# Performance work log

Hardware: AMD Instinct MI355X
Metric: run time of the kernel (lower is better)

## Reference

```python
import jax, jax.numpy as jnp
import numpy as np

DIM = 256
HEAD_DIM = 64
NH = DIM // HEAD_DIM
PS = 2  # fine patch size
EPS = 1e-5


def _conv(x, w, b, stride, pad):
    y = jax.lax.conv_general_dilated(x, w, (stride, stride), ((pad, pad), (pad, pad)),
                                     dimension_numbers=('NCHW', 'OIHW', 'NCHW'))
    return y + b[None, :, None, None]


def _bn(x, g, b, m, v):
    s = g * jax.lax.rsqrt(v + EPS)
    return x * s[None, :, None, None] + (b - m * s)[None, :, None, None]


def setup_inputs() -> dict:
    key = jax.random.key(0)
    ks = jax.random.split(key, 24)
    C = DIM
    d = {}
    d['x'] = jax.random.normal(ks[0], (8, C, 64, 64), jnp.float32)
    # Downsample conv (C->C, k=4, s=2, p=1), torch OIHW layout
    d['w_down'] = jax.random.normal(ks[1], (C, C, 4, 4), jnp.float32) * 0.02
    d['b_down'] = jax.random.normal(ks[2], (C,), jnp.float32) * 0.02
    # coarse to_qkv Linear(64 -> 192), stored as [in, out]
    d['w_qkv_c'] = jax.random.normal(ks[3], (HEAD_DIM, 3 * HEAD_DIM), jnp.float32) * 0.05
    d['b_qkv_c'] = jax.random.normal(ks[4], (3 * HEAD_DIM,), jnp.float32) * 0.02
    # Upsample ConvTranspose2d (torch [in, out, kH, kW] layout)
    d['w_up'] = jax.random.normal(ks[5], (C, C, 4, 4), jnp.float32) * 0.02
    d['b_up'] = jax.random.normal(ks[6], (C,), jnp.float32) * 0.02
    # fine to_qkv Linear(64 -> 192)
    d['w_qkv_f'] = jax.random.normal(ks[7], (HEAD_DIM, 3 * HEAD_DIM), jnp.float32) * 0.05
    d['b_qkv_f'] = jax.random.normal(ks[8], (3 * HEAD_DIM,), jnp.float32) * 0.02
    # DWConv: depthwise 3x3 (groups=C) -> BN -> relu6 -> pointwise 1x1 -> BN -> relu6
    d['w_dw'] = jax.random.normal(ks[9], (C, 1, 3, 3), jnp.float32) * 0.1
    d['bn_dw_g'] = jax.random.uniform(ks[10], (C,), jnp.float32) * 0.5 + 0.75
    d['bn_dw_b'] = jax.random.normal(ks[11], (C,), jnp.float32) * 0.1
    d['bn_dw_m'] = jax.random.normal(ks[12], (C,), jnp.float32) * 0.1
    d['bn_dw_v'] = jax.random.uniform(ks[13], (C,), jnp.float32) + 0.5
    d['w_pw'] = jax.random.normal(ks[14], (C, C, 1, 1), jnp.float32) * 0.05
    d['bn_pw_g'] = jax.random.uniform(ks[15], (C,), jnp.float32) * 0.5 + 0.75
    d['bn_pw_b'] = jax.random.normal(ks[16], (C,), jnp.float32) * 0.1
    d['bn_pw_m'] = jax.random.normal(ks[17], (C,), jnp.float32) * 0.1
    d['bn_pw_v'] = jax.random.uniform(ks[18], (C,), jnp.float32) + 0.5
    return d


def reference(x, w_down, b_down, w_qkv_c, b_qkv_c, w_up, b_up, w_qkv_f, b_qkv_f,
              w_dw, bn_dw_g, bn_dw_b, bn_dw_m, bn_dw_v,
              w_pw, bn_pw_g, bn_pw_b, bn_pw_m, bn_pw_v):
    B, C, H, W = x.shape
    nh, hd = C // HEAD_DIM, HEAD_DIM
    scale = hd ** -0.5

    # ---- CoarseSelfAttention ----
    xd = _conv(x, w_down, b_down, 2, 1)           # [B,C,h,w]
    h, w = xd.shape[2], xd.shape[3]
    P = h * w
    tok = xd.reshape(B, nh, hd, P).transpose(0, 1, 3, 2)   # [B,nh,P,hd]
    q, k, v = jnp.split(tok @ w_qkv_c + b_qkv_c, 3, axis=-1)
    attn = jax.nn.softmax(jnp.einsum('bhqd,bhkd->bhqk', q, k) * scale, axis=-1)
    coarse_score = attn.sum(axis=-2)               # [B,nh,P]
    kf = max(1, P // 4)
    top_k = jax.lax.top_k(coarse_score, kf)[1]     # [B,nh,kf]
    out = jnp.einsum('bhqk,bhkd->bhqd', attn, v)
    out = out.transpose(0, 1, 3, 2).reshape(B, C, h, w)
    # ConvTranspose2d(k=4,s=2,p=1) as lhs-dilated conv with flipped/transposed kernel
    wt = jnp.flip(w_up, (2, 3)).transpose(1, 0, 2, 3)
    coarse = jax.lax.conv_general_dilated(out, wt, (1, 1), ((2, 2), (2, 2)),
                                          lhs_dilation=(2, 2),
                                          dimension_numbers=('NCHW', 'OIHW', 'NCHW'))
    coarse = coarse + b_up[None, :, None, None]
    # F.interpolate to (H,W) is identity here: upsample exactly restores HxW

    # ---- TopkSelfAttention ----
    ph, pw = H // PS, W // PS                      # ph*pw == P
    xh = coarse.reshape(B, nh, hd, ph, PS, pw, PS)
    patches = xh.transpose(0, 1, 2, 3, 5, 4, 6).reshape(B, nh, hd, ph * pw, PS, PS)
    idx = jnp.broadcast_to(top_k[:, :, None, :, None, None], (B, nh, hd, kf, PS, PS))
    sel = jnp.take_along_axis(patches, idx, axis=3)        # [B,nh,hd,kf,PS,PS]
    tokf = sel.reshape(B, nh, hd, kf, PS * PS).transpose(0, 1, 3, 4, 2)
    tokf = tokf.reshape(B, nh, kf * PS * PS, hd)
    qf, kk, vf = jnp.split(tokf @ w_qkv_f + b_qkv_f, 3, axis=-1)
    attnf = jax.nn.softmax(jnp.einsum('bhqd,bhkd->bhqk', qf, kk) * scale, axis=-1)
    outf = jnp.einsum('bhqk,bhkd->bhqd', attnf, vf)
    outf = outf.reshape(B, nh, kf, PS * PS, hd).transpose(0, 1, 2, 4, 3)
    outf = outf.reshape(B, nh, kf, hd, PS, PS)     # [B,nh,kf,hd,PS,PS]
    # scatter selected patches back into zeros (topk indices are unique per b,h)
    res = jnp.zeros((B, nh, ph * pw, hd, PS, PS), x.dtype)
    bi = jnp.arange(B)[:, None, None]
    hi = jnp.arange(nh)[None, :, None]
    res = res.at[bi, hi, top_k].set(outf)
    res = res.transpose(0, 1, 3, 2, 4, 5).reshape(B, nh, hd, ph, pw, PS, PS)
    region = res.transpose(0, 1, 2, 3, 5, 4, 6).reshape(B, C, H, W)

    y = coarse + region

    # ---- DWConv feed-forward ----
    yd = jax.lax.conv_general_dilated(y, w_dw, (1, 1), ((1, 1), (1, 1)),
                                      feature_group_count=C,
                                      dimension_numbers=('NCHW', 'OIHW', 'NCHW'))
    yd = jnp.clip(_bn(yd, bn_dw_g, bn_dw_b, bn_dw_m, bn_dw_v), 0.0, 6.0)
    yp = jax.lax.conv_general_dilated(yd, w_pw, (1, 1), ((0, 0), (0, 0)),
                                      dimension_numbers=('NCHW', 'OIHW', 'NCHW'))
    yp = jnp.clip(_bn(yp, bn_pw_g, bn_pw_b, bn_pw_m, bn_pw_v), 0.0, 6.0)
    return yp
```

## Files before the change

### kernel.cpp

```cpp
#include <hip/hip_runtime.h>
#include <cstdint>
#include <cstddef>


#define EPS_ 1e-5f

typedef short bf16x8_t __attribute__((ext_vector_type(8)));
typedef float f32x4_t __attribute__((ext_vector_type(4)));
#define MFMA16(a, b, c) __builtin_amdgcn_mfma_f32_16x16x32_bf16(a, b, c, 0, 0, 0)

__device__ __forceinline__ void cvt1(float f, unsigned short& h, unsigned short& l) {
  unsigned u = __float_as_uint(f);
  unsigned r = u + 0x7FFFu + ((u >> 16) & 1u);
  h = (unsigned short)(r >> 16);
  float lo = f - __uint_as_float(r & 0xFFFF0000u);
  l = (unsigned short)(__float_as_uint(lo) >> 16);
}
__device__ __forceinline__ unsigned cvtpack(float f) {
  unsigned short h, l;
  cvt1(f, h, l);
  return (unsigned)h | ((unsigned)l << 16);
}
__device__ __forceinline__ void cvt2(float f0, float f1, unsigned& hpack, unsigned& lpack) {
  unsigned u0 = __float_as_uint(f0), u1 = __float_as_uint(f1);
  unsigned r0 = u0 + 0x7FFFu + ((u0 >> 16) & 1u);
  unsigned r1 = u1 + 0x7FFFu + ((u1 >> 16) & 1u);
  hpack = (r0 >> 16) | (r1 & 0xFFFF0000u);
  float l0 = f0 - __uint_as_float(r0 & 0xFFFF0000u);
  float l1 = f1 - __uint_as_float(r1 & 0xFFFF0000u);
  lpack = (__float_as_uint(l0) >> 16) | (__float_as_uint(l1) & 0xFFFF0000u);
}
__device__ __forceinline__ unsigned pk_h(unsigned a, unsigned b) {
  return (a & 0xFFFFu) | (b << 16);
}
__device__ __forceinline__ unsigned pk_l(unsigned a, unsigned b) {
  return (a >> 16) | (b & 0xFFFF0000u);
}

__global__ __launch_bounds__(256) void k_pad_x(
    const float* __restrict__ x, unsigned* __restrict__ xphl) {
  const int plane = blockIdx.x;
  const float* src = x + (size_t)plane * 4096;
  unsigned* dst = xphl + (size_t)plane * 4488;
  for (int e = threadIdx.x; e < 4356; e += 256) {
    int r = e / 66, cc = e - r * 66;
    float v = 0.f;
    if (r >= 1 && r <= 64 && cc >= 1 && cc <= 64) v = src[(r - 1) * 64 + (cc - 1)];
    dst[r * 68 + cc] = cvtpack(v);
  }
}

__global__ __launch_bounds__(256) void k_cvt_wdown(
    const float* __restrict__ w, unsigned short* __restrict__ wh,
    unsigned short* __restrict__ wl) {
  int e = blockIdx.x * 256 + threadIdx.x;
  cvt1(w[e], wh[e], wl[e]);
}

__global__ __launch_bounds__(256) void k_cvt_wqkv(
    const float* __restrict__ wq, unsigned short* __restrict__ wh,
    unsigned short* __restrict__ wl) {
  int e = blockIdx.x * 256 + threadIdx.x;
  int col = e >> 6, d = e & 63;
  float f = wq[d * 192 + col];
  if (col < 64) f *= 0.125f;
  cvt1(f, wh[e], wl[e]);
}

__global__ __launch_bounds__(256) void k_cvt_wup(
    const float* __restrict__ w_up, unsigned short* __restrict__ wth,
    unsigned short* __restrict__ wtl) {
  int e = blockIdx.x * 256 + threadIdx.x;
  int kp = e & 1023, oc = (e >> 10) & 255, c = e >> 18;
  int tap = kp >> 8, ic = kp & 255;
  int tk = tap >> 1, txi = tap & 1;
  int ry = c >> 1, rx = c & 1;
  int ky = (1 - ry) + 2 * tk, kx = (1 - rx) + 2 * txi;
  cvt1(w_up[((size_t)(ic * 256 + oc) * 4 + ky) * 4 + kx], wth[e], wtl[e]);
}

__global__ __launch_bounds__(256) void k_cvt_wpw(
    const float* __restrict__ w, unsigned short* __restrict__ wh,
    unsigned short* __restrict__ wl) {
  int e = blockIdx.x * 256 + threadIdx.x;
  cvt1(w[e], wh[e], wl[e]);
}

__device__ __forceinline__ void mfma_chunk(
    const unsigned short (*Ah)[72], const unsigned short (*Al)[72],
    const unsigned short (*Bh)[72], const unsigned short (*Bl)[72],
    f32x4_t (&acc)[4], int wm, int lane) {
  const int l16 = lane & 15, quad = lane >> 4;
#pragma unroll
  for (int ks = 0; ks < 2; ++ks) {
    int ko = ks * 32 + quad * 8;
    bf16x8_t ah = *(const bf16x8_t*)&Ah[wm + l16][ko];
    bf16x8_t al = *(const bf16x8_t*)&Al[wm + l16][ko];
#pragma unroll
    for (int nt = 0; nt < 4; ++nt) {
      bf16x8_t bh = *(const bf16x8_t*)&Bh[nt * 16 + l16][ko];
      bf16x8_t bl = *(const bf16x8_t*)&Bl[nt * 16 + l16][ko];
      acc[nt] = MFMA16(ah, bh, acc[nt]);
      acc[nt] = MFMA16(ah, bl, acc[nt]);
      acc[nt] = MFMA16(al, bh, acc[nt]);
    }
  }
}

__device__ __forceinline__ void mfma_chunk_regB(
    const unsigned short (*Ah)[72], const unsigned short (*Al)[72],
    const bf16x8_t (&bh)[2][4], const bf16x8_t (&bl)[2][4],
    f32x4_t (&acc)[4], int wm, int lane) {
  const int l16 = lane & 15, quad = lane >> 4;
#pragma unroll
  for (int ks = 0; ks < 2; ++ks) {
    int ko = ks * 32 + quad * 8;
    bf16x8_t ah = *(const bf16x8_t*)&Ah[wm + l16][ko];
    bf16x8_t al = *(const bf16x8_t*)&Al[wm + l16][ko];
#pragma unroll
    for (int nt = 0; nt < 4; ++nt) {
      acc[nt] = MFMA16(ah, bh[ks][nt], acc[nt]);
      acc[nt] = MFMA16(ah, bl[ks][nt], acc[nt]);
      acc[nt] = MFMA16(al, bh[ks][nt], acc[nt]);
    }
  }
}

__device__ __forceinline__ void mfma_tile2x2(
    const unsigned short (*Ah)[72], const unsigned short (*Al)[72],
    const unsigned short (*Bh)[72], const unsigned short (*Bl)[72],
    f32x4_t (&acc)[2][2], int wm, int wn, int lane) {
  const int l16 = lane & 15, quad = lane >> 4;
#pragma unroll
  for (int ks = 0; ks < 2; ++ks) {
    int ko = ks * 32 + quad * 8;
    bf16x8_t ah[2], al[2];
#pragma unroll
    for (int mt = 0; mt < 2; ++mt) {
      ah[mt] = *(const bf16x8_t*)&Ah[wm + mt * 16 + l16][ko];
      al[mt] = *(const bf16x8_t*)&Al[wm + mt * 16 + l16][ko];
    }
#pragma unroll
    for (int nt = 0; nt < 2; ++nt) {
      bf16x8_t bh = *(const bf16x8_t*)&Bh[wn + nt * 16 + l16][ko];
      bf16x8_t bl = *(const bf16x8_t*)&Bl[wn + nt * 16 + l16][ko];
#pragma unroll
      for (int mt = 0; mt < 2; ++mt) {
        acc[mt][nt] = MFMA16(ah[mt], bh, acc[mt][nt]);
        acc[mt][nt] = MFMA16(ah[mt], bl, acc[mt][nt]);
        acc[mt][nt] = MFMA16(al[mt], bh, acc[mt][nt]);
      }
    }
  }
}

__device__ __forceinline__ void mfma_tile2x4(
    const unsigned short (*Ah)[72], const unsigned short (*Al)[72],
    const unsigned short (*Bh)[72], const unsigned short (*Bl)[72],
    f32x4_t (&acc)[2][4], int wm, int wn, int lane) {
  const int l16 = lane & 15, quad = lane >> 4;
#pragma unroll
  for (int ks = 0; ks < 2; ++ks) {
    int ko = ks * 32 + quad * 8;
    bf16x8_t ah[2], al[2];
#pragma unroll
    for (int mt = 0; mt < 2; ++mt) {
      ah[mt] = *(const bf16x8_t*)&Ah[wm + mt * 16 + l16][ko];
      al[mt] = *(const bf16x8_t*)&Al[wm + mt * 16 + l16][ko];
    }
#pragma unroll
    for (int nt = 0; nt < 4; ++nt) {
      bf16x8_t bh = *(const bf16x8_t*)&Bh[wn + nt * 16 + l16][ko];
      bf16x8_t bl = *(const bf16x8_t*)&Bl[wn + nt * 16 + l16][ko];
#pragma unroll
      for (int mt = 0; mt < 2; ++mt) {
        acc[mt][nt] = MFMA16(ah[mt], bh, acc[mt][nt]);
        acc[mt][nt] = MFMA16(ah[mt], bl, acc[mt][nt]);
        acc[mt][nt] = MFMA16(al[mt], bh, acc[mt][nt]);
      }
    }
  }
}

__global__ __launch_bounds__(256) void k_conv_down_mfma(
    const unsigned* __restrict__ xphl, const unsigned short* __restrict__ wdh,
    const unsigned short* __restrict__ wdl, const float* __restrict__ bias,
    unsigned* __restrict__ xdhl) {
  __shared__ unsigned short Ah[64][72], Al[64][72], Bh[64][72], Bl[64][72];
  const int t = threadIdx.x;
  const int pix0 = blockIdx.x * 64, oc0 = blockIdx.y * 64;
  const int bimg = pix0 >> 10, pos = pix0 & 1023;
  const int pl = t & 63, icg = t >> 6;
  const int rem = (pix0 + pl) & 1023;
  const int oy = rem >> 5, ox = rem & 31;
  const unsigned* xb = xphl + ((size_t)bimg * 256 + icg) * 4488 + (oy * 2) * 68 + ox * 2;
  const int wave = t >> 6, lane = t & 63, l16 = lane & 15, quad = lane >> 4;
  const int wm = (wave & 1) * 32, wn = (wave >> 1) * 32;
  const int ar = t >> 2, ac = (t & 3) * 16;
  const unsigned short* wra = wdh + (size_t)(oc0 + ar) * 4096 + ac;
  const unsigned short* wrl = wdl + (size_t)(oc0 + ar) * 4096 + ac;
  f32x4_t acc[2][2] = {};
  bf16x8_t a0, a1, a2, a3;
  uint2 u01[4], u23[4];
  a0 = *(const bf16x8_t*)(wra);
  a1 = *(const bf16x8_t*)(wra + 8);
  a2 = *(const bf16x8_t*)(wrl);
  a3 = *(const bf16x8_t*)(wrl + 8);
#pragma unroll
  for (int r = 0; r < 4; ++r) {
    u01[r] = *(const uint2*)(xb + r * 68);
    u23[r] = *(const uint2*)(xb + r * 68 + 2);
  }
  for (int kb = 0; kb < 4096; kb += 64) {
    unsigned hp[8], lp[8];
#pragma unroll
    for (int r = 0; r < 4; ++r) {
      hp[2 * r]     = pk_h(u01[r].x, u01[r].y);
      lp[2 * r]     = pk_l(u01[r].x, u01[r].y);
      hp[2 * r + 1] = pk_h(u23[r].x, u23[r].y);
      lp[2 * r + 1] = pk_l(u23[r].x, u23[r].y);
    }
    __syncthreads();
    *(bf16x8_t*)&Ah[ar][ac] = a0;
    *(bf16x8_t*)&Ah[ar][ac + 8] = a1;
    *(bf16x8_t*)&Al[ar][ac] = a2;
    *(bf16x8_t*)&Al[ar][ac + 8] = a3;
    *(uint4*)&Bh[pl][icg * 16] = make_uint4(hp[0], hp[1], hp[2], hp[3]);
    *(uint4*)&Bh[pl][icg * 16 + 8] = make_uint4(hp[4], hp[5], hp[6], hp[7]);
    *(uint4*)&Bl[pl][icg * 16] = make_uint4(lp[0], lp[1], lp[2], lp[3]);
    *(uint4*)&Bl[pl][icg * 16 + 8] = make_uint4(lp[4], lp[5], lp[6], lp[7]);
    if (kb + 64 < 4096) {
      xb += 4 * 4488;
      a0 = *(const bf16x8_t*)(wra + kb + 64);
      a1 = *(const bf16x8_t*)(wra + kb + 64 + 8);
      a2 = *(const bf16x8_t*)(wrl + kb + 64);
      a3 = *(const bf16x8_t*)(wrl + kb + 64 + 8);
#pragma unroll
      for (int r = 0; r < 4; ++r) {
        u01[r] = *(const uint2*)(xb + r * 68);
        u23[r] = *(const uint2*)(xb + r * 68 + 2);
      }
    }
    __syncthreads();
    mfma_tile2x2(Ah, Al, Bh, Bl, acc, wm, wn, lane);
  }
#pragma unroll
  for (int mt = 0; mt < 2; ++mt)
#pragma unroll
    for (int r = 0; r < 4; ++r) {
      int oc = oc0 + wm + mt * 16 + quad * 4 + r;
      float bv = bias[oc];
#pragma unroll
      for (int nt = 0; nt < 2; ++nt)
        xdhl[((size_t)(bimg * 256 + oc)) * 1024 + pos + wn + nt * 16 + l16] =
            cvtpack(acc[mt][nt][r] + bv);
    }
}

template <int MODE>
__global__ __launch_bounds__(256) void k_qkv_mfma(
    const unsigned* __restrict__ srcp, const float* __restrict__ srcf,
    const unsigned short* __restrict__ wh, const unsigned short* __restrict__ wl,
    const float* __restrict__ bq, const int* __restrict__ topk,
    unsigned short* __restrict__ qh, unsigned short* __restrict__ ql,
    unsigned short* __restrict__ kh, unsigned short* __restrict__ kl,
    unsigned short* __restrict__ vth, unsigned short* __restrict__ vtl) {
  __shared__ unsigned short Ah[64][72], Al[64][72];
  const int t = threadIdx.x;
  const int tok0 = blockIdx.x * 64;
  const int pair = blockIdx.y;
  const int b = pair >> 2, h = pair & 3;
  const int tokl = t & 63, dg = t >> 6;
  unsigned hp[8], lp[8];
  if (MODE == 0) {
    const unsigned* base = srcp + ((size_t)(b * 256 + h * 64 + dg * 16)) * 1024 + tok0 + tokl;
    unsigned u[16];
#pragma unroll
    for (int j = 0; j < 16; ++j) u[j] = base[(size_t)j * 1024];
#pragma unroll
    for (int j = 0; j < 8; ++j) {
      hp[j] = pk_h(u[2 * j], u[2 * j + 1]);
      lp[j] = pk_l(u[2 * j], u[2 * j + 1]);
    }
  } else {
    int tok = tok0 + tokl;
    int pp = topk[pair * 256 + (tok >> 2)];
    int py = (tok >> 1) & 1, px = tok & 1;
    int ry = (pp >> 5) * 2 + py, rx = (pp & 31) * 2 + px;
    const float* base = srcf + ((size_t)(b * 256 + h * 64 + dg * 16)) * 4096 + ry * 64 + rx;
    float fv[16];
#pragma unroll
    for (int j = 0; j < 16; ++j) fv[j] = base[(size_t)j * 4096];
#pragma unroll
    for (int j = 0; j < 8; ++j) cvt2(fv[2 * j], fv[2 * j + 1], hp[j], lp[j]);
  }
  *(uint4*)&Ah[tokl][dg * 16] = make_uint4(hp[0], hp[1], hp[2], hp[3]);
  *(uint4*)&Ah[tokl][dg * 16 + 8] = make_uint4(hp[4], hp[5], hp[6], hp[7]);
  *(uint4*)&Al[tokl][dg * 16] = make_uint4(lp[0], lp[1], lp[2], lp[3]);
  *(uint4*)&Al[tokl][dg * 16 + 8] = make_uint4(lp[4], lp[5], lp[6], lp[7]);
  __syncthreads();
  const int wave = t >> 6, lane = t & 63, l16 = lane & 15, quad = lane >> 4;
  f32x4_t acc[4][3] = {};
#pragma unroll
  for (int ks = 0; ks < 2; ++ks) {
    int ko = ks * 32 + quad * 8;
    bf16x8_t bh0[3], bl0[3];
#pragma unroll
    for (int nt = 0; nt < 3; ++nt) {
      int col = wave * 48 + nt * 16 + l16;
      bh0[nt] = *(const bf16x8_t*)(wh + col * 64 + ko);
      bl0[nt] = *(const bf16x8_t*)(wl + col * 64 + ko);
    }
#pragma unroll
    for (int mt = 0; mt < 4; ++mt) {
      bf16x8_t ah = *(const bf16x8_t*)&Ah[mt * 16 + l16][ko];
      bf16x8_t al = *(const bf16x8_t*)&Al[mt * 16 + l16][ko];
#pragma unroll
      for (int nt = 0; nt < 3; ++nt) {
        acc[mt][nt] = MFMA16(ah, bh0[nt], acc[mt][nt]);
        acc[mt][nt] = MFMA16(ah, bl0[nt], acc[mt][nt]);
        acc[mt][nt] = MFMA16(al, bh0[nt], acc[mt][nt]);
      }
    }
  }
#pragma unroll
  for (int nt = 0; nt < 3; ++nt) {
    int col = wave * 48 + nt * 16 + l16;
    float bqv = bq[col];
    if (col < 64) bqv *= 0.125f;
#pragma unroll
    for (int mt = 0; mt < 4; ++mt) {
#pragma unroll
      for (int r = 0; r < 4; ++r) {
        int tok = tok0 + mt * 16 + quad * 4 + r;
        float val = acc[mt][nt][r] + bqv;
        unsigned short hh, ll;
        cvt1(val, hh, ll);
        if (col < 64) {
          size_t o = ((size_t)pair * 1024 + tok) * 64 + col;
          qh[o] = hh; ql[o] = ll;
        } else if (col < 128) {
          size_t o = ((size_t)pair * 1024 + tok) * 64 + (col - 64);
          kh[o] = hh; kl[o] = ll;
        } else {
          size_t o = ((size_t)pair * 64 + (col - 128)) * 1024 + tok;
          vth[o] = hh; vtl[o] = ll;
        }
      }
    }
  }
}

__global__ __launch_bounds__(256, 2) void k_attn_coarse(
    const unsigned short* __restrict__ qh, const unsigned short* __restrict__ ql,
    const unsigned short* __restrict__ kh, const unsigned short* __restrict__ kl,
    const unsigned short* __restrict__ vth, const unsigned short* __restrict__ vtl,
    float* __restrict__ score, unsigned* __restrict__ outc) {
  __shared__ __align__(16) unsigned short Kb[2][64][72];
  __shared__ __align__(16) unsigned short Vb[2][64][72];
  __shared__ __align__(16) unsigned short Pb[2][64][72];
  __shared__ float mlW[4][2][64];
  __shared__ float mC[64], lC[64];
  __shared__ float colsum[1024];
  const int t = threadIdx.x;
  const int q0 = blockIdx.x * 64;
  const int pair = blockIdx.y;
  const int wave = t >> 6, lane = t & 63;
  const int l16 = lane & 15, quad = lane >> 4;
  const int wm = wave * 16;
  const int sr = t >> 3, skc = (t & 7) * 8;

  const size_t qbase = ((size_t)pair * 1024 + q0) * 64;
  bf16x8_t qh_r[2][4], ql_r[2][4];
#pragma unroll
  for (int ks = 0; ks < 2; ++ks)
#pragma unroll
    for (int nt = 0; nt < 4; ++nt) {
      int row = nt * 16 + l16, col = ks * 32 + quad * 8;
      qh_r[ks][nt] = *(const bf16x8_t*)(qh + qbase + (size_t)row * 64 + col);
      ql_r[ks][nt] = *(const bf16x8_t*)(ql + qbase + (size_t)row * 64 + col);
    }
#pragma unroll
  for (int i = 0; i < 4; ++i) colsum[t + i * 256] = 0.f;

  const size_t kmbase = (size_t)pair * 1024 * 64;
  const size_t vbase = (size_t)pair * 64 * 1024;

  bf16x8_t pk0[2], pk1[2];
#pragma unroll
  for (int i = 0; i < 2; ++i) {
    int r = sr + i * 32;
    pk0[i] = *(const bf16x8_t*)(kh + kmbase + (size_t)r * 64 + skc);
    pk1[i] = *(const bf16x8_t*)(kl + kmbase + (size_t)r * 64 + skc);
  }

  float mrun[4] = {-1e30f, -1e30f, -1e30f, -1e30f};
  float lrun[4] = {0.f, 0.f, 0.f, 0.f};
// ... 141 lines not shown
    const unsigned short* __restrict__ kh, const unsigned short* __restrict__ kl,
    const unsigned short* __restrict__ vth, const unsigned short* __restrict__ vtl,
    float* __restrict__ outf) {
  __shared__ __align__(16) unsigned short Kb[2][64][72];
  __shared__ __align__(16) unsigned short Vb[2][64][72];
  __shared__ __align__(16) unsigned short Pb[2][64][72];
  __shared__ float m_run[64], l_run[64], alphaS[64];
  __shared__ float mWc[4][64], sWc[4][64];
  const int t = threadIdx.x;
  const int q0 = blockIdx.x * 64;
  const int pair = blockIdx.y;
  const int wave = t >> 6, lane = t & 63;
  const int l16 = lane & 15, quad = lane >> 4;
  const int wm = wave * 16;
  const int sr = t >> 3, skc = (t & 7) * 8;

  const size_t qbase = ((size_t)pair * 1024 + q0) * 64;
  bf16x8_t qh_r[2][4], ql_r[2][4];
#pragma unroll
  for (int ks = 0; ks < 2; ++ks)
#pragma unroll
    for (int nt = 0; nt < 4; ++nt) {
      int row = nt * 16 + l16, col = ks * 32 + quad * 8;
      qh_r[ks][nt] = *(const bf16x8_t*)(qh + qbase + (size_t)row * 64 + col);
      ql_r[ks][nt] = *(const bf16x8_t*)(ql + qbase + (size_t)row * 64 + col);
    }
  if (t < 64) { m_run[t] = -1e30f; l_run[t] = 0.f; }

  const size_t kmbase = (size_t)pair * 1024 * 64;
  const size_t vbase = (size_t)pair * 64 * 1024;

  bf16x8_t pk0[2], pk1[2], pv0[2], pv1[2];
#pragma unroll
  for (int i = 0; i < 2; ++i) {
    int r = sr + i * 32;
    pk0[i] = *(const bf16x8_t*)(kh + kmbase + (size_t)r * 64 + skc);
    pk1[i] = *(const bf16x8_t*)(kl + kmbase + (size_t)r * 64 + skc);
    pv0[i] = *(const bf16x8_t*)(vth + vbase + (size_t)r * 1024 + skc);
    pv1[i] = *(const bf16x8_t*)(vtl + vbase + (size_t)r * 1024 + skc);
  }

  f32x4_t accO[4] = {};
  for (int kb = 0; kb < 1024; kb += 64) {
    __syncthreads();
#pragma unroll
    for (int i = 0; i < 2; ++i) {
      int r = sr + i * 32;
      *(bf16x8_t*)&Kb[0][r][skc] = pk0[i];
      *(bf16x8_t*)&Kb[1][r][skc] = pk1[i];
      *(bf16x8_t*)&Vb[0][r][skc] = pv0[i];
      *(bf16x8_t*)&Vb[1][r][skc] = pv1[i];
    }
    if (kb + 64 < 1024) {
#pragma unroll
      for (int i = 0; i < 2; ++i) {
        int r = sr + i * 32;
        pk0[i] = *(const bf16x8_t*)(kh + kmbase + (size_t)(kb + 64 + r) * 64 + skc);
        pk1[i] = *(const bf16x8_t*)(kl + kmbase + (size_t)(kb + 64 + r) * 64 + skc);
        pv0[i] = *(const bf16x8_t*)(vth + vbase + (size_t)r * 1024 + kb + 64 + skc);
        pv1[i] = *(const bf16x8_t*)(vtl + vbase + (size_t)r * 1024 + kb + 64 + skc);
      }
    }
    __syncthreads();
    f32x4_t acc[4] = {};
    mfma_chunk_regB(Kb[0], Kb[1], qh_r, ql_r, acc, wm, lane);
#pragma unroll
    for (int nt = 0; nt < 4; ++nt) {
      float m0 = fmaxf(fmaxf(acc[nt][0], acc[nt][1]), fmaxf(acc[nt][2], acc[nt][3]));
      m0 = fmaxf(m0, __shfl_xor(m0, 16));
      m0 = fmaxf(m0, __shfl_xor(m0, 32));
      if (quad == 0) mWc[wave][nt * 16 + l16] = m0;
    }
    __syncthreads();
    if (t < 64) {
      float mn = fmaxf(fmaxf(fmaxf(mWc[0][t], mWc[1][t]), fmaxf(mWc[2][t], mWc[3][t])),
                       m_run[t]);
      alphaS[t] = __expf(m_run[t] - mn);
      m_run[t] = mn;
    }
    __syncthreads();
    float P[4][4];
#pragma unroll
    for (int nt = 0; nt < 4; ++nt) {
      float mn = m_run[nt * 16 + l16];
#pragma unroll
      for (int r = 0; r < 4; ++r) P[nt][r] = __expf(acc[nt][r] - mn);
      float s0 = P[nt][0] + P[nt][1] + P[nt][2] + P[nt][3];
      s0 += __shfl_xor(s0, 16);
      s0 += __shfl_xor(s0, 32);
      if (quad == 0) sWc[wave][nt * 16 + l16] = s0;
      unsigned h01, l01, h23, l23;
      cvt2(P[nt][0], P[nt][1], h01, l01);
      cvt2(P[nt][2], P[nt][3], h23, l23);
      *(uint2*)&Pb[0][nt * 16 + l16][wm + quad * 4] = make_uint2(h01, h23);
      *(uint2*)&Pb[1][nt * 16 + l16][wm + quad * 4] = make_uint2(l01, l23);
    }
#pragma unroll
    for (int r = 0; r < 4; ++r) {
      float a = alphaS[wm + quad * 4 + r];
#pragma unroll
      for (int nt = 0; nt < 4; ++nt) accO[nt][r] *= a;
    }
    __syncthreads();
    if (t < 64)
      l_run[t] = l_run[t] * alphaS[t] + (sWc[0][t] + sWc[1][t] + sWc[2][t] + sWc[3][t]);
    mfma_chunk(Pb[0], Pb[1], Vb[0], Vb[1], accO, wm, lane);
  }
  __syncthreads();
#pragma unroll
  for (int r = 0; r < 4; ++r) {
    float invl = 1.0f / l_run[wm + quad * 4 + r];
    int qm = q0 + wm + quad * 4 + r;
#pragma unroll
    for (int nt = 0; nt < 4; ++nt)
      outf[((size_t)pair * 1024 + qm) * 64 + nt * 16 + l16] = accO[nt][r] * invl;
  }
}

__global__ __launch_bounds__(256) void k_topk(
    const float* __restrict__ score, int* __restrict__ idx) {
  __shared__ unsigned long long key[1024];
  const int pair = blockIdx.x;
  const int t = threadIdx.x;
#pragma unroll
  for (int j = 0; j < 4; ++j) {
    int i = t + j * 256;
    unsigned u = __float_as_uint(score[pair * 1024 + i]);
    u = u ^ ((u & 0x80000000u) ? 0xFFFFFFFFu : 0x80000000u);
    u = ~u;
    key[i] = ((unsigned long long)u << 32) | (unsigned)i;
  }
  __syncthreads();
  for (int k = 2; k <= 1024; k <<= 1) {
    for (int j = k >> 1; j > 0; j >>= 1) {
      for (int w = 0; w < 4; ++w) {
        int i = t + w * 256;
        int l = i ^ j;
        if (l > i) {
          bool up = ((i & k) == 0);
          unsigned long long a = key[i], b = key[l];
          if ((a > b) == up) { key[i] = b; key[l] = a; }
        }
      }
      __syncthreads();
    }
  }
  idx[pair * 256 + t] = (int)(key[t] & 0xFFFFFFFFu);
}

__global__ __launch_bounds__(256) void k_convT_mfma(
    const unsigned* __restrict__ inp, const unsigned short* __restrict__ wth,
    const unsigned short* __restrict__ wtl, const float* __restrict__ bias,
    float* __restrict__ out) {
  __shared__ unsigned short Ah[64][72], Al[64][72];
  __shared__ unsigned short Bh[128][72], Bl[128][72];
  const int t = threadIdx.x;
  const int pix0 = blockIdx.x * 128;
  const int oc0 = blockIdx.y * 64;
  const int cls = blockIdx.z;
  const int ry = cls >> 1, rx = cls & 1;
  const int b = pix0 >> 10;
  const int wave = t >> 6, lane = t & 63;
  const int l16 = lane & 15, quad = lane >> 4;
  const int wm = (wave & 1) * 32, wn = (wave >> 1) * 64;
  const int pl = t & 127, icg = t >> 7;
  const int remg = (pix0 + pl) & 1023;
  const int tyy = remg >> 5, txx = remg & 31;
  const int ar = t >> 2, ac = (t & 3) * 16;
  const size_t wbase = ((size_t)cls * 256 + oc0 + ar) * 1024 + ac;
  f32x4_t acc[2][4] = {};
  bf16x8_t a0, a1, a2, a3;
  unsigned u[32];
  {
    const int iy = tyy + ry + 1, ix = txx + rx + 1;
    const unsigned* p = inp + (size_t)(b * 256 + icg * 32) * 1156 + iy * 34 + ix;
#pragma unroll
    for (int j = 0; j < 32; ++j) u[j] = p[(size_t)j * 1156];
    a0 = *(const bf16x8_t*)(wth + wbase);
    a1 = *(const bf16x8_t*)(wth + wbase + 8);
    a2 = *(const bf16x8_t*)(wtl + wbase);
    a3 = *(const bf16x8_t*)(wtl + wbase + 8);
  }
  for (int kb = 0; kb < 1024; kb += 64) {
    unsigned hp[16], lpk[16];
#pragma unroll
    for (int j = 0; j < 16; ++j) {
      hp[j] = pk_h(u[2 * j], u[2 * j + 1]);
      lpk[j] = pk_l(u[2 * j], u[2 * j + 1]);
    }
    __syncthreads();
    *(bf16x8_t*)&Ah[ar][ac] = a0;
    *(bf16x8_t*)&Ah[ar][ac + 8] = a1;
    *(bf16x8_t*)&Al[ar][ac] = a2;
    *(bf16x8_t*)&Al[ar][ac + 8] = a3;
    {
      int kc = icg * 32;
      *(uint4*)&Bh[pl][kc] = make_uint4(hp[0], hp[1], hp[2], hp[3]);
      *(uint4*)&Bh[pl][kc + 8] = make_uint4(hp[4], hp[5], hp[6], hp[7]);
      *(uint4*)&Bh[pl][kc + 16] = make_uint4(hp[8], hp[9], hp[10], hp[11]);
      *(uint4*)&Bh[pl][kc + 24] = make_uint4(hp[12], hp[13], hp[14], hp[15]);
      *(uint4*)&Bl[pl][kc] = make_uint4(lpk[0], lpk[1], lpk[2], lpk[3]);
      *(uint4*)&Bl[pl][kc + 8] = make_uint4(lpk[4], lpk[5], lpk[6], lpk[7]);
      *(uint4*)&Bl[pl][kc + 16] = make_uint4(lpk[8], lpk[9], lpk[10], lpk[11]);
      *(uint4*)&Bl[pl][kc + 24] = make_uint4(lpk[12], lpk[13], lpk[14], lpk[15]);
    }
    if (kb + 64 < 1024) {
      const int kn = kb + 64;
      const int tap = kn >> 8, ic0 = kn & 255;
      const int tk = tap >> 1, txi = tap & 1;
      const int iy = tyy + ry + 1 - tk, ix = txx + rx + 1 - txi;
      const unsigned* p = inp + (size_t)(b * 256 + ic0 + icg * 32) * 1156 + iy * 34 + ix;
#pragma unroll
      for (int j = 0; j < 32; ++j) u[j] = p[(size_t)j * 1156];
      a0 = *(const bf16x8_t*)(wth + wbase + kn);
      a1 = *(const bf16x8_t*)(wth + wbase + kn + 8);
      a2 = *(const bf16x8_t*)(wtl + wbase + kn);
      a3 = *(const bf16x8_t*)(wtl + wbase + kn + 8);
    }
    __syncthreads();
    mfma_tile2x4(Ah, Al, Bh, Bl, acc, wm, wn, lane);
  }
#pragma unroll
  for (int mt = 0; mt < 2; ++mt)
#pragma unroll
    for (int r = 0; r < 4; ++r) {
      int oc = oc0 + wm + mt * 16 + quad * 4 + r;
      float bvs = bias[oc];
#pragma unroll
      for (int nt = 0; nt < 4; ++nt) {
        int pix = pix0 + wn + nt * 16 + l16;
        int rem2 = pix & 1023;
        int y = (rem2 >> 5) * 2 + ry, xx = (rem2 & 31) * 2 + rx;
        out[((size_t)(b * 256 + oc) * 64 + y) * 64 + xx] = acc[mt][nt][r] + bvs;
      }
    }
}

__global__ __launch_bounds__(256) void k_scatter(
    const float* __restrict__ outf, const int* __restrict__ idx,
    float* __restrict__ y) {
  int g = blockIdx.x * 256 + threadIdx.x;
  int pair = g >> 16;
  int rem = g & 65535;
  int tok = rem >> 6, d = rem & 63;
  int b = pair >> 2, h = pair & 3;
  int pp = idx[pair * 256 + (tok >> 2)];
  int py = (tok >> 1) & 1, px = tok & 1;
  int ry = (pp >> 5) * 2 + py, rx = (pp & 31) * 2 + px;
  y[((size_t)(b * 256 + h * 64 + d) * 64 + ry) * 64 + rx] += outf[g];
}

__global__ __launch_bounds__(256) void k_dwconv(
    const float* __restrict__ y, const float* __restrict__ wdw,
    const float* __restrict__ g, const float* __restrict__ bb,
    const float* __restrict__ m, const float* __restrict__ vv,
    unsigned* __restrict__ ydhl) {
  int gi = blockIdx.x * 256 + threadIdx.x;
  int x = gi & 63, yy = (gi >> 6) & 63, ch = (gi >> 12) & 255, b = gi >> 20;
  const float* plane = y + (size_t)(b * 256 + ch) * 4096;
  const float* wc = wdw + ch * 9;
  float s = 0.f;
#pragma unroll
  for (int ky = 0; ky < 3; ++ky) {
    int iy = yy + ky - 1;
    if (iy < 0 || iy >= 64) continue;
#pragma unroll
    for (int kx = 0; kx < 3; ++kx) {
      int ix = x + kx - 1;
      if (ix < 0 || ix >= 64) continue;
      s = fmaf(plane[iy * 64 + ix], wc[ky * 3 + kx], s);
    }
  }
  float sc = g[ch] * rsqrtf(vv[ch] + EPS_);
  float val = s * sc + (bb[ch] - m[ch] * sc);
  ydhl[gi] = cvtpack(fminf(fmaxf(val, 0.f), 6.f));
}

__global__ __launch_bounds__(256) void k_pw_mfma(
    const unsigned* __restrict__ ydhl, const unsigned short* __restrict__ wh,
    const unsigned short* __restrict__ wl, const float* __restrict__ g,
    const float* __restrict__ bb, const float* __restrict__ m,
    const float* __restrict__ vv, float* __restrict__ out) {
  __shared__ unsigned short Ah[64][72], Al[64][72];
  __shared__ unsigned short Bh[128][72], Bl[128][72];
  const int t = threadIdx.x;
  const int pix0 = blockIdx.x * 128;
  const int oc0 = blockIdx.y * 64;
  const int b = pix0 >> 12, pos0 = pix0 & 4095;
  const int wave = t >> 6, lane = t & 63;
  const int l16 = lane & 15, quad = lane >> 4;
  const int wm = (wave & 1) * 32, wn = (wave >> 1) * 64;
  const int pl = t & 127, icg = t >> 7;
  const int ar = t >> 2, ac = (t & 3) * 16;
  f32x4_t acc[2][4] = {};
  bf16x8_t a0, a1, a2, a3;
  unsigned u[32];
  {
    const unsigned* p = ydhl + (size_t)(b * 256 + icg * 32) * 4096 + pos0 + pl;
#pragma unroll
    for (int j = 0; j < 32; ++j) u[j] = p[(size_t)j * 4096];
    a0 = *(const bf16x8_t*)(wh + (size_t)(oc0 + ar) * 256 + ac);
    a1 = *(const bf16x8_t*)(wh + (size_t)(oc0 + ar) * 256 + ac + 8);
    a2 = *(const bf16x8_t*)(wl + (size_t)(oc0 + ar) * 256 + ac);
    a3 = *(const bf16x8_t*)(wl + (size_t)(oc0 + ar) * 256 + ac + 8);
  }
  for (int kb = 0; kb < 256; kb += 64) {
    unsigned hp[16], lpk[16];
#pragma unroll
    for (int j = 0; j < 16; ++j) {
      hp[j] = pk_h(u[2 * j], u[2 * j + 1]);
      lpk[j] = pk_l(u[2 * j], u[2 * j + 1]);
    }
    __syncthreads();
    *(bf16x8_t*)&Ah[ar][ac] = a0;
    *(bf16x8_t*)&Ah[ar][ac + 8] = a1;
    *(bf16x8_t*)&Al[ar][ac] = a2;
    *(bf16x8_t*)&Al[ar][ac + 8] = a3;
    {
      int kc = icg * 32;
      *(uint4*)&Bh[pl][kc] = make_uint4(hp[0], hp[1], hp[2], hp[3]);
      *(uint4*)&Bh[pl][kc + 8] = make_uint4(hp[4], hp[5], hp[6], hp[7]);
      *(uint4*)&Bh[pl][kc + 16] = make_uint4(hp[8], hp[9], hp[10], hp[11]);
      *(uint4*)&Bh[pl][kc + 24] = make_uint4(hp[12], hp[13], hp[14], hp[15]);
      *(uint4*)&Bl[pl][kc] = make_uint4(lpk[0], lpk[1], lpk[2], lpk[3]);
      *(uint4*)&Bl[pl][kc + 8] = make_uint4(lpk[4], lpk[5], lpk[6], lpk[7]);
      *(uint4*)&Bl[pl][kc + 16] = make_uint4(lpk[8], lpk[9], lpk[10], lpk[11]);
      *(uint4*)&Bl[pl][kc + 24] = make_uint4(lpk[12], lpk[13], lpk[14], lpk[15]);
    }
    if (kb + 64 < 256) {
      const int kn = kb + 64;
      const unsigned* p = ydhl + (size_t)(b * 256 + kn + icg * 32) * 4096 + pos0 + pl;
#pragma unroll
      for (int j = 0; j < 32; ++j) u[j] = p[(size_t)j * 4096];
      a0 = *(const bf16x8_t*)(wh + (size_t)(oc0 + ar) * 256 + kn + ac);
      a1 = *(const bf16x8_t*)(wh + (size_t)(oc0 + ar) * 256 + kn + ac + 8);
      a2 = *(const bf16x8_t*)(wl + (size_t)(oc0 + ar) * 256 + kn + ac);
      a3 = *(const bf16x8_t*)(wl + (size_t)(oc0 + ar) * 256 + kn + ac + 8);
    }
    __syncthreads();
    mfma_tile2x4(Ah, Al, Bh, Bl, acc, wm, wn, lane);
  }
#pragma unroll
  for (int mt = 0; mt < 2; ++mt)
#pragma unroll
    for (int r = 0; r < 4; ++r) {
      int oc = oc0 + wm + mt * 16 + quad * 4 + r;
      float sc = g[oc] * rsqrtf(vv[oc] + EPS_);
      float off = bb[oc] - m[oc] * sc;
#pragma unroll
      for (int nt = 0; nt < 4; ++nt) {
        int pix = pos0 + wn + nt * 16 + l16;
        float val = fminf(fmaxf(acc[mt][nt][r] * sc + off, 0.f), 6.f);
        out[(size_t)(b * 256 + oc) * 4096 + pix] = val;
      }
    }
}

extern "C" void kernel_launch(void* const* d_in, const int* in_sizes, int n_in,
                              void* d_out, int out_size, void* d_ws, size_t ws_size,
                              hipStream_t stream) {
  (void)in_sizes; (void)n_in; (void)out_size; (void)ws_size;
  const float* x       = (const float*)d_in[0];
  const float* w_down  = (const float*)d_in[1];
  const float* b_down  = (const float*)d_in[2];
  const float* w_qkv_c = (const float*)d_in[3];
  const float* b_qkv_c = (const float*)d_in[4];
  const float* w_up    = (const float*)d_in[5];
  const float* b_up    = (const float*)d_in[6];
  const float* w_qkv_f = (const float*)d_in[7];
  const float* b_qkv_f = (const float*)d_in[8];
  const float* w_dw    = (const float*)d_in[9];
  const float* bn_dw_g = (const float*)d_in[10];
  const float* bn_dw_b = (const float*)d_in[11];
  const float* bn_dw_m = (const float*)d_in[12];
  const float* bn_dw_v = (const float*)d_in[13];
  const float* w_pw    = (const float*)d_in[14];
  const float* bn_pw_g = (const float*)d_in[15];
  const float* bn_pw_b = (const float*)d_in[16];
  const float* bn_pw_m = (const float*)d_in[17];
  const float* bn_pw_v = (const float*)d_in[18];

  float* ws = (float*)d_ws;
  unsigned*       xphl   = (unsigned*)ws;
  unsigned*       ydhl   = (unsigned*)ws;
  unsigned short* qh     = (unsigned short*)(ws + 33554432);
  unsigned short* ql     = (unsigned short*)(ws + 34603008);
  unsigned short* kh     = (unsigned short*)(ws + 35651584);
  unsigned short* kl     = (unsigned short*)(ws + 36700160);
  unsigned short* vth    = (unsigned short*)(ws + 37748736);
  unsigned short* vtl    = (unsigned short*)(ws + 38797312);
  unsigned*       xdhl   = (unsigned*)(ws + 39845888);
  unsigned*       outcphl= (unsigned*)(ws + 41943040);
  float*          coarse = ws + 44310528;
  float*          outf   = ws + 52699136;
  float*          score  = ws + 54796288;
  unsigned short* wdh    = (unsigned short*)(ws + 54829056);
  unsigned short* wdl    = (unsigned short*)(ws + 55353344);
  unsigned short* wt_hi  = (unsigned short*)(ws + 55877632);
  unsigned short* wt_lo  = (unsigned short*)(ws + 56401920);
  unsigned short* wpw_hi = (unsigned short*)(ws + 56926208);
  unsigned short* wpw_lo = (unsigned short*)(ws + 56958976);
  unsigned short* wqh_c  = (unsigned short*)(ws + 56991744);
  unsigned short* wql_c  = (unsigned short*)(ws + 56997888);
  unsigned short* wqh_f  = (unsigned short*)(ws + 57004032);
  unsigned short* wql_f  = (unsigned short*)(ws + 57010176);
  int*            idx    = (int*)(ws + 57016320);

  hipMemsetAsync(score, 0, 32768 * sizeof(float), stream);
  hipMemsetAsync(outcphl, 0, (size_t)2367488 * sizeof(unsigned), stream);
  k_pad_x<<<2048, 256, 0, stream>>>(x, xphl);
  k_cvt_wdown<<<4096, 256, 0, stream>>>(w_down, wdh, wdl);
  k_cvt_wqkv<<<48, 256, 0, stream>>>(w_qkv_c, wqh_c, wql_c);
  k_cvt_wqkv<<<48, 256, 0, stream>>>(w_qkv_f, wqh_f, wql_f);
  k_cvt_wup<<<4096, 256, 0, stream>>>(w_up, wt_hi, wt_lo);
  k_cvt_wpw<<<256, 256, 0, stream>>>(w_pw, wpw_hi, wpw_lo);

  k_conv_down_mfma<<<dim3(128, 4), 256, 0, stream>>>(xphl, wdh, wdl, b_down, xdhl);
  k_qkv_mfma<0><<<dim3(16, 32), 256, 0, stream>>>(xdhl, nullptr, wqh_c, wql_c, b_qkv_c,
                                                  nullptr, qh, ql, kh, kl, vth, vtl);
  k_attn_coarse<<<dim3(16, 32), 256, 0, stream>>>(qh, ql, kh, kl, vth, vtl, score, outcphl);
  k_topk<<<32, 256, 0, stream>>>(score, idx);
  k_convT_mfma<<<dim3(64, 4, 4), 256, 0, stream>>>(outcphl, wt_hi, wt_lo, b_up, coarse);

  k_qkv_mfma<1><<<dim3(16, 32), 256, 0, stream>>>(nullptr, coarse, wqh_f, wql_f, b_qkv_f,
                                                  idx, qh, ql, kh, kl, vth, vtl);
  k_attn_fine<<<dim3(16, 32), 256, 0, stream>>>(qh, ql, kh, kl, vth, vtl, outf);
  k_scatter<<<8192, 256, 0, stream>>>(outf, idx, coarse);
  k_dwconv<<<32768, 256, 0, stream>>>(coarse, w_dw, bn_dw_g, bn_dw_b, bn_dw_m, bn_dw_v, ydhl);
  k_pw_mfma<<<dim3(256, 4), 256, 0, stream>>>(ydhl, wpw_hi, wpw_lo, bn_pw_g, bn_pw_b,
                                              bn_pw_m, bn_pw_v, (float*)d_out);
}
```

Measured before the change: 598.7 us.

## Double-buffer LDS in MFMA conv GEMMs and shrink convT/pointwise pixel tiles

Converts the down-conv, transposed-conv and pointwise-conv GEMM loops to ping-pong shared-memory buffers, removing one barrier per k-step. ConvT and pointwise kernels also drop from 128-pixel to 64-pixel tiles with 2x2 MFMA per wave, doubling grid size and reducing registers. The trade is higher LDS usage per block and less operand reuse per tile.

```diff
diff --git a/kernel.cpp b/kernel.cpp
--- a/kernel.cpp
+++ b/kernel.cpp
@@ -154,39 +154,12 @@
   }
 }
 
-__device__ __forceinline__ void mfma_tile2x4(
-    const unsigned short (*Ah)[72], const unsigned short (*Al)[72],
-    const unsigned short (*Bh)[72], const unsigned short (*Bl)[72],
-    f32x4_t (&acc)[2][4], int wm, int wn, int lane) {
-  const int l16 = lane & 15, quad = lane >> 4;
-#pragma unroll
-  for (int ks = 0; ks < 2; ++ks) {
-    int ko = ks * 32 + quad * 8;
-    bf16x8_t ah[2], al[2];
-#pragma unroll
-    for (int mt = 0; mt < 2; ++mt) {
-      ah[mt] = *(const bf16x8_t*)&Ah[wm + mt * 16 + l16][ko];
-      al[mt] = *(const bf16x8_t*)&Al[wm + mt * 16 + l16][ko];
-    }
-#pragma unroll
-    for (int nt = 0; nt < 4; ++nt) {
-      bf16x8_t bh = *(const bf16x8_t*)&Bh[wn + nt * 16 + l16][ko];
-      bf16x8_t bl = *(const bf16x8_t*)&Bl[wn + nt * 16 + l16][ko];
-#pragma unroll
-      for (int mt = 0; mt < 2; ++mt) {
-        acc[mt][nt] = MFMA16(ah[mt], bh, acc[mt][nt]);
-        acc[mt][nt] = MFMA16(ah[mt], bl, acc[mt][nt]);
-        acc[mt][nt] = MFMA16(al[mt], bh, acc[mt][nt]);
-      }
-    }
-  }
-}
-
 __global__ __launch_bounds__(256) void k_conv_down_mfma(
     const unsigned* __restrict__ xphl, const unsigned short* __restrict__ wdh,
     const unsigned short* __restrict__ wdl, const float* __restrict__ bias,
     unsigned* __restrict__ xdhl) {
-  __shared__ unsigned short Ah[64][72], Al[64][72], Bh[64][72], Bl[64][72];
+  __shared__ unsigned short Ah[2][64][72], Al[2][64][72];
+  __shared__ unsigned short Bh[2][64][72], Bl[2][64][72];
   const int t = threadIdx.x;
   const int pix0 = blockIdx.x * 64, oc0 = blockIdx.y * 64;
   const int bimg = pix0 >> 10, pos = pix0 & 1023;
@@ -211,6 +184,7 @@
     u01[r] = *(const uint2*)(xb + r * 68);
     u23[r] = *(const uint2*)(xb + r * 68 + 2);
   }
+  int cur = 0;
   for (int kb = 0; kb < 4096; kb += 64) {
     unsigned hp[8], lp[8];
 #pragma unroll
@@ -220,15 +194,14 @@
       hp[2 * r + 1] = pk_h(u23[r].x, u23[r].y);
       lp[2 * r + 1] = pk_l(u23[r].x, u23[r].y);
     }
-    __syncthreads();
-    *(bf16x8_t*)&Ah[ar][ac] = a0;
-    *(bf16x8_t*)&Ah[ar][ac + 8] = a1;
-    *(bf16x8_t*)&Al[ar][ac] = a2;
-    *(bf16x8_t*)&Al[ar][ac + 8] = a3;
-    *(uint4*)&Bh[pl][icg * 16] = make_uint4(hp[0], hp[1], hp[2], hp[3]);
-    *(uint4*)&Bh[pl][icg * 16 + 8] = make_uint4(hp[4], hp[5], hp[6], hp[7]);
-    *(uint4*)&Bl[pl][icg * 16] = make_uint4(lp[0], lp[1], lp[2], lp[3]);
-    *(uint4*)&Bl[pl][icg * 16 + 8] = make_uint4(lp[4], lp[5], lp[6], lp[7]);
+    *(bf16x8_t*)&Ah[cur][ar][ac] = a0;
+    *(bf16x8_t*)&Ah[cur][ar][ac + 8] = a1;
+    *(bf16x8_t*)&Al[cur][ar][ac] = a2;
+    *(bf16x8_t*)&Al[cur][ar][ac + 8] = a3;
+    *(uint4*)&Bh[cur][pl][icg * 16] = make_uint4(hp[0], hp[1], hp[2], hp[3]);
+    *(uint4*)&Bh[cur][pl][icg * 16 + 8] = make_uint4(hp[4], hp[5], hp[6], hp[7]);
+    *(uint4*)&Bl[cur][pl][icg * 16] = make_uint4(lp[0], lp[1], lp[2], lp[3]);
+    *(uint4*)&Bl[cur][pl][icg * 16 + 8] = make_uint4(lp[4], lp[5], lp[6], lp[7]);
     if (kb + 64 < 4096) {
       xb += 4 * 4488;
       a0 = *(const bf16x8_t*)(wra + kb + 64);
@@ -242,7 +215,8 @@
       }
     }
     __syncthreads();
-    mfma_tile2x2(Ah, Al, Bh, Bl, acc, wm, wn, lane);
+    mfma_tile2x2(Ah[cur], Al[cur], Bh[cur], Bl[cur], acc, wm, wn, lane);
+    cur ^= 1;
   }
 #pragma unroll
   for (int mt = 0; mt < 2; ++mt)
@@ -690,73 +664,67 @@
     const unsigned* __restrict__ inp, const unsigned short* __restrict__ wth,
     const unsigned short* __restrict__ wtl, const float* __restrict__ bias,
     float* __restrict__ out) {
-  __shared__ unsigned short Ah[64][72], Al[64][72];
-  __shared__ unsigned short Bh[128][72], Bl[128][72];
+  __shared__ unsigned short Ah[2][64][72], Al[2][64][72];
+  __shared__ unsigned short Bh[2][64][72], Bl[2][64][72];
   const int t = threadIdx.x;
-  const int pix0 = blockIdx.x * 128;
+  const int pix0 = blockIdx.x * 64;
   const int oc0 = blockIdx.y * 64;
   const int cls = blockIdx.z;
   const int ry = cls >> 1, rx = cls & 1;
   const int b = pix0 >> 10;
   const int wave = t >> 6, lane = t & 63;
   const int l16 = lane & 15, quad = lane >> 4;
-  const int wm = (wave & 1) * 32, wn = (wave >> 1) * 64;
-  const int pl = t & 127, icg = t >> 7;
+  const int wm = (wave & 1) * 32, wn = (wave >> 1) * 32;
+  const int pl = t & 63, icg = t >> 6;
   const int remg = (pix0 + pl) & 1023;
   const int tyy = remg >> 5, txx = remg & 31;
   const int ar = t >> 2, ac = (t & 3) * 16;
   const size_t wbase = ((size_t)cls * 256 + oc0 + ar) * 1024 + ac;
-  f32x4_t acc[2][4] = {};
+  f32x4_t acc[2][2] = {};
   bf16x8_t a0, a1, a2, a3;
-  unsigned u[32];
+  unsigned u[16];
   {
     const int iy = tyy + ry + 1, ix = txx + rx + 1;
-    const unsigned* p = inp + (size_t)(b * 256 + icg * 32) * 1156 + iy * 34 + ix;
-#pragma unroll
-    for (int j = 0; j < 32; ++j) u[j] = p[(size_t)j * 1156];
+    const unsigned* p = inp + (size_t)(b * 256 + icg * 16) * 1156 + iy * 34 + ix;
+#pragma unroll
+    for (int j = 0; j < 16; ++j) u[j] = p[(size_t)j * 1156];
     a0 = *(const bf16x8_t*)(wth + wbase);
     a1 = *(const bf16x8_t*)(wth + wbase + 8);
     a2 = *(const bf16x8_t*)(wtl + wbase);
     a3 = *(const bf16x8_t*)(wtl + wbase + 8);
   }
+  int cur = 0;
   for (int kb = 0; kb < 1024; kb += 64) {
-    unsigned hp[16], lpk[16];
-#pragma unroll
-    for (int j = 0; j < 16; ++j) {
+    unsigned hp[8], lpk[8];
+#pragma unroll
+    for (int j = 0; j < 8; ++j) {
       hp[j] = pk_h(u[2 * j], u[2 * j + 1]);
       lpk[j] = pk_l(u[2 * j], u[2 * j + 1]);
     }
-    __syncthreads();
-    *(bf16x8_t*)&Ah[ar][ac] = a0;
-    *(bf16x8_t*)&Ah[ar][ac + 8] = a1;
-    *(bf16x8_t*)&Al[ar][ac] = a2;
-    *(bf16x8_t*)&Al[ar][ac + 8] = a3;
-    {
-      int kc = icg * 32;
-      *(uint4*)&Bh[pl][kc] = make_uint4(hp[0], hp[1], hp[2], hp[3]);
-      *(uint4*)&Bh[pl][kc + 8] = make_uint4(hp[4], hp[5], hp[6], hp[7]);
-      *(uint4*)&Bh[pl][kc + 16] = make_uint4(hp[8], hp[9], hp[10], hp[11]);
-      *(uint4*)&Bh[pl][kc + 24] = make_uint4(hp[12], hp[13], hp[14], hp[15]);
-      *(uint4*)&Bl[pl][kc] = make_uint4(lpk[0], lpk[1], lpk[2], lpk[3]);
-      *(uint4*)&Bl[pl][kc + 8] = make_uint4(lpk[4], lpk[5], lpk[6], lpk[7]);
-      *(uint4*)&Bl[pl][kc + 16] = make_uint4(lpk[8], lpk[9], lpk[10], lpk[11]);
-      *(uint4*)&Bl[pl][kc + 24] = make_uint4(lpk[12], lpk[13], lpk[14], lpk[15]);
-    }
+    *(bf16x8_t*)&Ah[cur][ar][ac] = a0;
+    *(bf16x8_t*)&Ah[cur][ar][ac + 8] = a1;
+    *(bf16x8_t*)&Al[cur][ar][ac] = a2;
+    *(bf16x8_t*)&Al[cur][ar][ac + 8] = a3;
+    *(uint4*)&Bh[cur][pl][icg * 16] = make_uint4(hp[0], hp[1], hp[2], hp[3]);
+    *(uint4*)&Bh[cur][pl][icg * 16 + 8] = make_uint4(hp[4], hp[5], hp[6], hp[7]);
+    *(uint4*)&Bl[cur][pl][icg * 16] = make_uint4(lpk[0], lpk[1], lpk[2], lpk[3]);
+    *(uint4*)&Bl[cur][pl][icg * 16 + 8] = make_uint4(lpk[4], lpk[5], lpk[6], lpk[7]);
     if (kb + 64 < 1024) {
       const int kn = kb + 64;
       const int tap = kn >> 8, ic0 = kn & 255;
       const int tk = tap >> 1, txi = tap & 1;
       const int iy = tyy + ry + 1 - tk, ix = txx + rx + 1 - txi;
-      const unsigned* p = inp + (size_t)(b * 256 + ic0 + icg * 32) * 1156 + iy * 34 + ix;
-#pragma unroll
-      for (int j = 0; j < 32; ++j) u[j] = p[(size_t)j * 1156];
+      const unsigned* p = inp + (size_t)(b * 256 + ic0 + icg * 16) * 1156 + iy * 34 + ix;
+#pragma unroll
+      for (int j = 0; j < 16; ++j) u[j] = p[(size_t)j * 1156];
       a0 = *(const bf16x8_t*)(wth + wbase + kn);
       a1 = *(const bf16x8_t*)(wth + wbase + kn + 8);
       a2 = *(const bf16x8_t*)(wtl + wbase + kn);
       a3 = *(const bf16x8_t*)(wtl + wbase + kn + 8);
     }
     __syncthreads();
-    mfma_tile2x4(Ah, Al, Bh, Bl, acc, wm, wn, lane);
+    mfma_tile2x2(Ah[cur], Al[cur], Bh[cur], Bl[cur], acc, wm, wn, lane);
+    cur ^= 1;
   }
 #pragma unroll
   for (int mt = 0; mt < 2; ++mt)
@@ -765,7 +733,7 @@
       int oc = oc0 + wm + mt * 16 + quad * 4 + r;
       float bvs = bias[oc];
 #pragma unroll
-      for (int nt = 0; nt < 4; ++nt) {
+      for (int nt = 0; nt < 2; ++nt) {
         int pix = pix0 + wn + nt * 16 + l16;
         int rem2 = pix & 1023;
         int y = (rem2 >> 5) * 2 + ry, xx = (rem2 & 31) * 2 + rx;
@@ -819,64 +787,58 @@
     const unsigned short* __restrict__ wl, const float* __restrict__ g,
     const float* __restrict__ bb, const float* __restrict__ m,
     const float* __restrict__ vv, float* __restrict__ out) {
-  __shared__ unsigned short Ah[64][72], Al[64][72];
-  __shared__ unsigned short Bh[128][72], Bl[128][72];
+  __shared__ unsigned short Ah[2][64][72], Al[2][64][72];
+  __shared__ unsigned short Bh[2][64][72], Bl[2][64][72];
   const int t = threadIdx.x;
-  const int pix0 = blockIdx.x * 128;
+  const int pix0 = blockIdx.x * 64;
   const int oc0 = blockIdx.y * 64;
   const int b = pix0 >> 12, pos0 = pix0 & 4095;
   const int wave = t >> 6, lane = t & 63;
   const int l16 = lane & 15, quad = lane >> 4;
-  const int wm = (wave & 1) * 32, wn = (wave >> 1) * 64;
-  const int pl = t & 127, icg = t >> 7;
+  const int wm = (wave & 1) * 32, wn = (wave >> 1) * 32;
+  const int pl = t & 63, icg = t >> 6;
   const int ar = t >> 2, ac = (t & 3) * 16;
-  f32x4_t acc[2][4] = {};
+  f32x4_t acc[2][2] = {};
   bf16x8_t a0, a1, a2, a3;
-  unsigned u[32];
+  unsigned u[16];
   {
-    const unsigned* p = ydhl + (size_t)(b * 256 + icg * 32) * 4096 + pos0 + pl;
-#pragma unroll
-    for (int j = 0; j < 32; ++j) u[j] = p[(size_t)j * 4096];
+    const unsigned* p = ydhl + (size_t)(b * 256 + icg * 16) * 4096 + pos0 + pl;
+#pragma unroll
+    for (int j = 0; j < 16; ++j) u[j] = p[(size_t)j * 4096];
     a0 = *(const bf16x8_t*)(wh + (size_t)(oc0 + ar) * 256 + ac);
     a1 = *(const bf16x8_t*)(wh + (size_t)(oc0 + ar) * 256 + ac + 8);
     a2 = *(const bf16x8_t*)(wl + (size_t)(oc0 + ar) * 256 + ac);
     a3 = *(const bf16x8_t*)(wl + (size_t)(oc0 + ar) * 256 + ac + 8);
   }
+  int cur = 0;
   for (int kb = 0; kb < 256; kb += 64) {
-    unsigned hp[16], lpk[16];
-#pragma unroll
-    for (int j = 0; j < 16; ++j) {
+    unsigned hp[8], lpk[8];
+#pragma unroll
+    for (int j = 0; j < 8; ++j) {
       hp[j] = pk_h(u[2 * j], u[2 * j + 1]);
       lpk[j] = pk_l(u[2 * j], u[2 * j + 1]);
     }
-    __syncthreads();
-    *(bf16x8_t*)&Ah[ar][ac] = a0;
-    *(bf16x8_t*)&Ah[ar][ac + 8] = a1;
-    *(bf16x8_t*)&Al[ar][ac] = a2;
-    *(bf16x8_t*)&Al[ar][ac + 8] = a3;
-    {
-      int kc = icg * 32;
-      *(uint4*)&Bh[pl][kc] = make_uint4(hp[0], hp[1], hp[2], hp[3]);
-      *(uint4*)&Bh[pl][kc + 8] = make_uint4(hp[4], hp[5], hp[6], hp[7]);
-      *(uint4*)&Bh[pl][kc + 16] = make_uint4(hp[8], hp[9], hp[10], hp[11]);
-      *(uint4*)&Bh[pl][kc + 24] = make_uint4(hp[12], hp[13], hp[14], hp[15]);
-      *(uint4*)&Bl[pl][kc] = make_uint4(lpk[0], lpk[1], lpk[2], lpk[3]);
-      *(uint4*)&Bl[pl][kc + 8] = make_uint4(lpk[4], lpk[5], lpk[6], lpk[7]);
-      *(uint4*)&Bl[pl][kc + 16] = make_uint4(lpk[8], lpk[9], lpk[10], lpk[11]);
-      *(uint4*)&Bl[pl][kc + 24] = make_uint4(lpk[12], lpk[13], lpk[14], lpk[15]);
-    }
+    *(bf16x8_t*)&Ah[cur][ar][ac] = a0;
+    *(bf16x8_t*)&Ah[cur][ar][ac + 8] = a1;
+    *(bf16x8_t*)&Al[cur][ar][ac] = a2;
+    *(bf16x8_t*)&Al[cur][ar][ac + 8] = a3;
+    *(uint4*)&Bh[cur][pl][icg * 16] = make_uint4(hp[0], hp[1], hp[2], hp[3]);
+    *(uint4*)&Bh[cur][pl][icg * 16 + 8] = make_uint4(hp[4], hp[5], hp[6], hp[7]);
+    *(uint4*)&Bl[cur][pl][icg * 16] = make_uint4(lpk[0], lpk[1], lpk[2], lpk[3]);
+    *(uint4*)&Bl[cur][pl][icg * 16 + 8] = make_uint4(lpk[4], lpk[5], lpk[6], lpk[7]);
     if (kb + 64 < 256) {
       const int kn = kb + 64;
-      const unsigned* p = ydhl + (size_t)(b * 256 + kn + icg * 32) * 4096 + pos0 + pl;
-#pragma unroll
-      for (int j = 0; j < 32; ++j) u[j] = p[(size_t)j * 4096];
+      const unsigned* p = ydhl + (size_t)(b * 256 + kn + icg * 16) * 4096 + pos0 + pl;
+#pragma unroll
+      for (int j = 0; j < 16; ++j) u[j] = p[(size_t)j * 4096];
       a0 = *(const bf16x8_t*)(wh + (size_t)(oc0 + ar) * 256 + kn + ac);
       a1 = *(const bf16x8_t*)(wh + (size_t)(oc0 + ar) * 256 + kn + ac + 8);
       a2 = *(const bf16x8_t*)(wl + (size_t)(oc0 + ar) * 256 + kn + ac);
       a3 = *(const bf16x8_t*)(wl + (size_t)(oc0 + ar) * 256 + kn + ac + 8);
     }
     __syncthreads();
-    mfma_tile2x4(Ah, Al, Bh, Bl, acc, wm, wn, lane);
+    mfma_tile2x2(Ah[cur], Al[cur], Bh[cur], Bl[cur], acc, wm, wn, lane);
+    cur ^= 1;
   }
 #pragma unroll
   for (int mt = 0; mt < 2; ++mt)
@@ -886,7 +848,7 @@
       float sc = g[oc] * rsqrtf(vv[oc] + EPS_);
       float off = bb[oc] - m[oc] * sc;
 #pragma unroll
-      for (int nt = 0; nt < 4; ++nt) {
+      for (int nt = 0; nt < 2; ++nt) {
         int pix = pos0 + wn + nt * 16 + l16;
         float val = fminf(fmaxf(acc[mt][nt][r] * sc + off, 0.f), 6.f);
         out[(size_t)(b * 256 + oc) * 4096 + pix] = val;
@@ -958,13 +920,13 @@
                                                   nullptr, qh, ql, kh, kl, vth, vtl);
   k_attn_coarse<<<dim3(16, 32), 256, 0, stream>>>(qh, ql, kh, kl, vth, vtl, score, outcphl);
   k_topk<<<32, 256, 0, stream>>>(score, idx);
-  k_convT_mfma<<<dim3(64, 4, 4), 256, 0, stream>>>(outcphl, wt_hi, wt_lo, b_up, coarse);
+  k_convT_mfma<<<dim3(128, 4, 4), 256, 0, stream>>>(outcphl, wt_hi, wt_lo, b_up, coarse);
 
   k_qkv_mfma<1><<<dim3(16, 32), 256, 0, stream>>>(nullptr, coarse, wqh_f, wql_f, b_qkv_f,
                                                   idx, qh, ql, kh, kl, vth, vtl);
   k_attn_fine<<<dim3(16, 32), 256, 0, stream>>>(qh, ql, kh, kl, vth, vtl, outf);
   k_scatter<<<8192, 256, 0, stream>>>(outf, idx, coarse);
   k_dwconv<<<32768, 256, 0, stream>>>(coarse, w_dw, bn_dw_g, bn_dw_b, bn_dw_m, bn_dw_v, ydhl);
-  k_pw_mfma<<<dim3(256, 4), 256, 0, stream>>>(ydhl, wpw_hi, wpw_lo, bn_pw_g, bn_pw_b,
+  k_pw_mfma<<<dim3(512, 4), 256, 0, stream>>>(ydhl, wpw_hi, wpw_lo, bn_pw_g, bn_pw_b,
                                               bn_pw_m, bn_pw_v, (float*)d_out);
 }
```

Measured after the change: 606.6 us. No clear change (+1.3%).
